# Kernel optimization log

Measured on AMD Instinct MI355X. Metric: run time of the kernel, lower is better.

The kernel has to match this reference:

```python
import jax, jax.numpy as jnp
import numpy as np

EPS = 1.0        # model eps for norm
STEP = 0.05      # step_size

def _norm(x):
    # torch: x / (eps + x.std(-1, keepdims=True)), torch std is unbiased (ddof=1)
    return x / (EPS + jnp.std(x, axis=-1, keepdims=True, ddof=1))

def setup_inputs() -> dict:
    key = jax.random.key(0)
    B, L, LM = 4, 512, 64
    G, E, K, D, KN = 32000, 256, 8, 6, 4
    ks = jax.random.split(key, 16)
    s = lambda k, shape, fan: (jax.random.normal(k, shape, jnp.float32) / np.sqrt(fan)).astype(jnp.float32)
    return dict(
        masked=jax.random.randint(ks[0], (B, L), 0, G),
        unmasked=jax.random.randint(ks[1], (B, L), 0, G),
        mask=jax.random.randint(ks[2], (B, LM), 0, L),
        embed=s(ks[3], (G, E), E),                 # embedding table
        Wt=s(ks[4], (D, E, E), E),                 # transition.weight per layer
        bt=jnp.zeros((D, E), jnp.float32),         # transition.bias per layer
        Wtc=s(ks[5], (D, E, E), E),                # transcore.weight per layer
        Wq=s(ks[6], (D, K * E, E), E),             # attq.weight per layer
        Wd=s(ks[7], (D, K * E, K * E), K * E),     # att_dense.weight per layer
        Wo=s(ks[8], (D, K * E, E), K * E),         # atto.weight per layer
        Wu=s(ks[9], (D, E, E), E),                 # updater.weight per layer
        Wem=s(ks[10], (E, E), E),                  # emittor.weight (head)
        Wkc=s(ks[11], (E * KN, E), E),             # kchoice.weight (head)
        bkc=jnp.zeros((E * KN,), jnp.float32),     # kchoice.bias (head)
    )

def reference(masked, unmasked, mask, embed, Wt, bt, Wtc, Wq, Wd, Wo, Wu, Wem, Wkc, bkc):
    B, L = masked.shape
    G, E = embed.shape
    K = Wq.shape[1] // E
    KN = Wkc.shape[0] // E
    inv_sqrt_e = 1.0 / np.sqrt(E)

    z = _norm(embed[masked])          # [B,L,E] input image
    xsa0 = z

    def step(xsa, p):
        wt, bt_, wtc, wq, wd, wo, wu = p
        # roll-based left/right transitions
        xsad = jax.nn.relu(jnp.roll(xsa, 1, axis=1) @ wt) @ wtc
        xsad = xsad + jax.nn.relu(jnp.roll(xsa, -1, axis=1) @ wtc.T) @ wt.T
        xsad = xsad + z @ wu.T + bt_   # use_input_image
        # QKV_Attention with kernel-expanded head dim: q [B,L,K,E] vs keys/values xsa [B,L,E]
        q = (xsa @ wq.T).reshape(B, L, K, E)
        h = jnp.einsum('blke,bme->blkm', q, xsa) * inv_sqrt_e
        pijk = jax.nn.softmax(h, axis=-1)
        y = jnp.einsum('blkm,bme->blke', pijk, xsa).reshape(B, L, K * E)
        # mode 1: Dense -> Relu -> Dense
        xid = jax.nn.relu(y @ wd.T) @ wo     # [B,L,E]
        xsad = _norm(xsad + xid)             # use_gradnorm
        xsa = _norm(xsa + STEP * xsad)       # use_layernorm
        return xsa, None

    xsa, _ = jax.lax.scan(step, xsa0, (Wt, bt, Wtc, Wq, Wd, Wo, Wu))

    # k-choice loss head (callback_cent)
    LM = mask.shape[1]
    lptok = jnp.take_along_axis(xsa, mask[:, :, None], axis=1)         # [B,LM,E]
    xx = (lptok @ Wkc.T + bkc).reshape(B, LM * KN, E)                  # kchoice
    xx = jnp.einsum('bnl,ble->bne', jnp.einsum('bne,ble->bnl', xx, xsa), xsa)
    logits = (xx @ Wem) @ embed.T                                      # [B,LM*KN,G]
    k_lp = jax.nn.log_softmax(logits, axis=-1).reshape(B, LM, KN, G)
    lptok = jax.scipy.special.logsumexp(k_lp, axis=2) - jnp.log(jnp.float32(KN))
    tgt = jnp.take_along_axis(unmasked, mask, axis=1)                  # [B,LM]
    cent = jnp.take_along_axis(lptok, tgt[:, :, None], axis=-1)[:, :, 0]
    return -cent.mean(-1)                                              # [B]
```

## Files before the change

kernel.cpp:

```cpp
#include <hip/hip_runtime.h>
#include <hip/hip_bf16.h>
#include <math.h>

typedef __bf16 bf16x8 __attribute__((ext_vector_type(8)));
typedef float floatx4 __attribute__((ext_vector_type(4)));

__device__ __forceinline__ short f2b(float f) {
  __hip_bfloat16 h = __float2bfloat16(f);
  return *reinterpret_cast<short*>(&h);
}
__device__ __forceinline__ float b2f(short s) {
  unsigned u = ((unsigned)(unsigned short)s) << 16;
  float f;
  __builtin_memcpy(&f, &u, 4);
  return f;
}

__device__ __forceinline__ void gl2lds16(const void* g, void* l) {
  __builtin_amdgcn_global_load_lds((__attribute__((address_space(1))) const void*)g,
                                   (__attribute__((address_space(3))) void*)l, 16, 0, 0);
}

__device__ __forceinline__ float block_sum(float v, float* sdata) {
#pragma unroll
  for (int o = 32; o > 0; o >>= 1) v += __shfl_down(v, o, 64);
  __syncthreads();
  int lane = threadIdx.x & 63, wid = threadIdx.x >> 6;
  if (lane == 0) sdata[wid] = v;
  __syncthreads();
  float s = 0.f;
  int nw = blockDim.x >> 6;
  for (int i = 0; i < nw; i++) s += sdata[i];
  return s;
}

__global__ void cvt_kernel(const float* __restrict__ src, short* __restrict__ dst, long n4) {
  long i = (long)blockIdx.x * blockDim.x + threadIdx.x;
  if (i < n4) {
    float4 v = ((const float4*)src)[i];
    short4 o;
    o.x = f2b(v.x); o.y = f2b(v.y); o.z = f2b(v.z); o.w = f2b(v.w);
    ((short4*)dst)[i] = o;
  }
}

__global__ void cvt2_kernel(const float* __restrict__ src, short* __restrict__ dst,
                            int ldS, int ldD, long sS, long sD) {
  src += (size_t)blockIdx.z * sS;
  dst += (size_t)blockIdx.z * sD;
  int c = blockIdx.x * 32 + threadIdx.x;
  int r0 = blockIdx.y * 32 + threadIdx.y;
#pragma unroll
  for (int i = 0; i < 32; i += 8)
    dst[(size_t)(r0 + i) * ldD + c] = f2b(src[(size_t)(r0 + i) * ldS + c]);
}

__global__ void cvtT2_kernel(const float* __restrict__ src, short* __restrict__ dst,
                             int ldS, int ldD, long sS, long sD) {
  src += (size_t)blockIdx.z * sS;
  dst += (size_t)blockIdx.z * sD;
  __shared__ float tile[32][33];
  int r0 = blockIdx.y * 32, c0 = blockIdx.x * 32;
  int tx = threadIdx.x, ty = threadIdx.y;
#pragma unroll
  for (int i = 0; i < 32; i += 8)
    tile[ty + i][tx] = src[(size_t)(r0 + ty + i) * ldS + c0 + tx];
  __syncthreads();
#pragma unroll
  for (int i = 0; i < 32; i += 8)
    dst[(size_t)(c0 + ty + i) * ldD + r0 + tx] = f2b(tile[tx][ty + i]);
}

__global__ void embed_norm_kernel(const int* __restrict__ masked,
                                  const float* __restrict__ embed,
                                  float* __restrict__ xsa, short* __restrict__ xsa_bf,
                                  short* __restrict__ xsaT_bf, short* __restrict__ catA,
                                  int E, int L, int ldA, int zoff) {
  int row = blockIdx.x;
  int g = masked[row];
  __shared__ float sdata[8];
  float x = embed[(size_t)g * E + threadIdx.x];
  float mean = block_sum(x, sdata) / E;
  float d = x - mean;
  float var = block_sum(d * d, sdata) / (E - 1);
  float val = x / (1.0f + sqrtf(var));
  size_t off = (size_t)row * E + threadIdx.x;
  xsa[off] = val;
  short b = f2b(val);
  xsa_bf[off] = b;
  catA[(size_t)row * ldA + zoff + threadIdx.x] = b;
  int bb = row / L, l = row - bb * L;
  xsaT_bf[((size_t)bb * E + threadIdx.x) * L + l] = b;
}

template <int BM, int BN, int OUT_BF16, int ASUM>
__global__ __launch_bounds__(256) void bgemm_kernel(
    const short* __restrict__ A, int lda, long sA,
    const short* __restrict__ B, int ldb, long sB,
    void* __restrict__ Cv, int ldc, long sC,
    short* __restrict__ C2b, int ldc2, int ncut,
    int Ksz, float alpha, const float* __restrict__ bias,
    int relu, int expo, int shiftA, int shiftB, int ns1, int ns2, int Lroll,
    int ksplit, long ksC) {
  constexpr int WM = BM / 2, WN = BN / 2;
  constexpr int MT = WM / 16, NT = WN / 16;
  constexpr int NCH = (BM + BN) * 8;
  constexpr int LPT = NCH / 256;
  int bz = blockIdx.z, kz = 0;
  if (ksplit > 1) {
    bz = blockIdx.z / ksplit;
    kz = blockIdx.z - bz * ksplit;
  }
  int Kper = Ksz / ksplit;
  int koff = kz * Kper;
  A += (size_t)bz * sA + koff;
  B += (size_t)bz * sB + koff;
  float* Cf = (float*)Cv + (size_t)bz * sC + (size_t)kz * ksC;
  short* Cb = (short*)Cv + (size_t)bz * sC;
  int m0 = blockIdx.y * BM, n0 = blockIdx.x * BN;
  int shift = (n0 < ns1) ? shiftA : ((n0 < ns2) ? shiftB : 0);
  int zone2 = (C2b != nullptr) && (n0 >= ncut);
  __shared__ short S[2][(BM + BN) * 64];
  int tid = threadIdx.x, lane = tid & 63, w = tid >> 6;
  int wm = (w & 1) * WM, wn = (w >> 1) * WN;
  int ml = lane & 15, q4 = lane >> 4, sw = ml & 7;

  const short* src[LPT];
#pragma unroll
  for (int i = 0; i < LPT; i++) {
    int q = i * 256 + w * 64 + lane;
    if (q < BM * 8) {
      int m = q >> 3, cl = q & 7, cs = cl ^ (m & 7);
      int mg = m0 + m;
      if (shift != 0) {
        int bb = mg / Lroll, l = mg - bb * Lroll;
        l = (l + shift + Lroll) % Lroll;
        mg = bb * Lroll + l;
      }
      src[i] = A + (size_t)mg * lda + cs * 8;
    } else {
      int qb = q - BM * 8;
      int n = qb >> 3, cl = qb & 7, cs = cl ^ (n & 7);
      src[i] = B + (size_t)(n0 + n) * ldb + cs * 8;
    }
  }
#pragma unroll
  for (int i = 0; i < LPT; i++)
    gl2lds16(src[i], &S[0][(i * 256 + w * 64) * 8]);
  floatx4 acc[MT][NT] = {};
  floatx4 sumacc[ASUM ? MT : 1] = {};
  bf16x8 ones;
#pragma unroll
  for (int i = 0; i < 8; i++) ones[i] = (__bf16)1.0f;
  int nT = Kper >> 6;
  for (int t = 0; t < nT; t++) {
    __syncthreads();
    int cur = t & 1;
    if (t + 1 < nT) {
      int nxt = cur ^ 1, ko = (t + 1) * 64;
#pragma unroll
      for (int i = 0; i < LPT; i++)
        gl2lds16(src[i] + ko, &S[nxt][(i * 256 + w * 64) * 8]);
    }
#pragma unroll
    for (int kk = 0; kk < 2; kk++) {
      int j = kk * 4 + q4;
      bf16x8 af[MT], bg[NT];
#pragma unroll
      for (int mt = 0; mt < MT; mt++) {
        int r = wm + mt * 16 + ml;
        af[mt] = *reinterpret_cast<const bf16x8*>(&S[cur][r * 64 + (j ^ sw) * 8]);
      }
#pragma unroll
      for (int nt = 0; nt < NT; nt++) {
        int r = wn + nt * 16 + ml;
        bg[nt] = *reinterpret_cast<const bf16x8*>(&S[cur][BM * 64 + r * 64 + (j ^ sw) * 8]);
      }
#pragma unroll
      for (int mt = 0; mt < MT; mt++)
#pragma unroll
        for (int nt = 0; nt < NT; nt++)
          acc[mt][nt] = __builtin_amdgcn_mfma_f32_16x16x32_bf16(af[mt], bg[nt], acc[mt][nt], 0, 0, 0);
      if (ASUM)
#pragma unroll
        for (int mt = 0; mt < MT; mt++)
          sumacc[mt] = __builtin_amdgcn_mfma_f32_16x16x32_bf16(af[mt], ones, sumacc[mt], 0, 0, 0);
    }
  }
#pragma unroll
  for (int mt = 0; mt < MT; mt++) {
    float sinv[4];
    if (ASUM) {
#pragma unroll
      for (int r = 0; r < 4; r++) sinv[r] = 1.f / sumacc[mt][r];
    }
#pragma unroll
    for (int nt = 0; nt < NT; nt++) {
      floatx4 v = acc[mt][nt];
#pragma unroll
      for (int r = 0; r < 4; r++) {
        int grow = m0 + wm + mt * 16 + q4 * 4 + r;
        int gcol = n0 + wn + nt * 16 + ml;
        float x = alpha * v[r];
        if (ASUM) x *= sinv[r];
        if (bias && kz == 0) x += bias[gcol];
        if (relu && !zone2) x = fmaxf(x, 0.f);
        if (expo) x = exp2f(x);
        if (OUT_BF16) {
          if (zone2)
            C2b[(size_t)grow * ldc2 + (gcol - ncut)] = f2b(x);
          else
            Cb[(size_t)grow * ldc + gcol] = f2b(x);
        } else {
          Cf[(size_t)grow * ldc + gcol] = x;
        }
      }
    }
  }
}

__global__ void addnorm_kernel(const float* __restrict__ xA, const float* __restrict__ xB,
                               float* __restrict__ xsa, short* __restrict__ xsa_bf,
                               short* __restrict__ xsaT_bf, int E, int L) {
  int row = blockIdx.x, t = threadIdx.x;
  __shared__ float sdata[8];
  size_t off = (size_t)row * E + t;
  float s1 = xA[off] + xB[off];
  float mean = block_sum(s1, sdata) / E;
  float d = s1 - mean;
  float var = block_sum(d * d, sdata) / (E - 1);
  float n1 = s1 / (1.f + sqrtf(var));
  float t2 = xsa[off] + 0.05f * n1;
  float mean2 = block_sum(t2, sdata) / E;
  float d2 = t2 - mean2;
  float var2 = block_sum(d2 * d2, sdata) / (E - 1);
  float res = t2 / (1.f + sqrtf(var2));
  xsa[off] = res;
  short b = f2b(res);
  xsa_bf[off] = b;
  int bb = row / L, l = row - bb * L;
  xsaT_bf[((size_t)bb * E + t) * L + l] = b;
}

__global__ void gather_kernel(const float* __restrict__ xsa, const int* __restrict__ mask,
                              const int* __restrict__ unmasked,
                              short* __restrict__ lptok_bf, int* __restrict__ tgt,
                              int L, int LM, int E) {
  int bi = blockIdx.x;
  int b = bi / LM;
  int pos = mask[bi];
  float v = xsa[((size_t)b * L + pos) * E + threadIdx.x];
  lptok_bf[(size_t)bi * E + threadIdx.x] = f2b(v);
  if (threadIdx.x == 0) tgt[bi] = unmasked[b * L + pos];
}

__global__ __launch_bounds__(256) void head_stats_kernel(
    const short* __restrict__ V, const short* __restrict__ Eb,
    float* __restrict__ stM, float* __restrict__ stS, int Ksz, int nch) {
  int t0 = blockIdx.x;
  int xcd = t0 & 7, j = t0 >> 3;
  int c = ((j >> 3) << 3) | xcd;
  if (c >= nch) return;
  int m0 = (j & 7) * 128, n0 = c * 128;
  __shared__ short As[2][8192];
  __shared__ short Bs[2][8192];
  int tid = threadIdx.x, lane = tid & 63, w = tid >> 6;
  int wm = (w & 1) * 64, wn = (w >> 1) * 64;
  int ml = lane & 15, q4 = lane >> 4, sw = ml & 7;
  const short* aSrc[4];
  const short* bSrc[4];
#pragma unroll
  for (int i = 0; i < 4; i++) {
    int q = i * 256 + w * 64 + lane;
    int m = q >> 3, cl = q & 7;
    int cs = cl ^ (m & 7);
    aSrc[i] = V + (size_t)(m0 + m) * Ksz + cs * 8;
    bSrc[i] = Eb + (size_t)(n0 + m) * Ksz + cs * 8;
  }
#pragma unroll
  for (int i = 0; i < 4; i++) {
    gl2lds16(aSrc[i], &As[0][(i * 256 + w * 64) * 8]);
    gl2lds16(bSrc[i], &Bs[0][(i * 256 + w * 64) * 8]);
  }
  floatx4 acc[4][4] = {};
  int nT = Ksz >> 6;
  for (int t = 0; t < nT; t++) {
    __syncthreads();
    int cur = t & 1;
    if (t + 1 < nT) {
      int nxt = cur ^ 1, ko = (t + 1) * 64;
#pragma unroll
      for (int i = 0; i < 4; i++) {
        gl2lds16(aSrc[i] + ko, &As[nxt][(i * 256 + w * 64) * 8]);
        gl2lds16(bSrc[i] + ko, &Bs[nxt][(i * 256 + w * 64) * 8]);
      }
    }
#pragma unroll
    for (int kk = 0; kk < 2; kk++) {
      int j2 = kk * 4 + q4;
      bf16x8 af[4], bg[4];
#pragma unroll
      for (int mt = 0; mt < 4; mt++) {
        int r = wm + mt * 16 + ml;
        af[mt] = *reinterpret_cast<const bf16x8*>(&As[cur][r * 64 + (j2 ^ sw) * 8]);
      }
#pragma unroll
      for (int nt = 0; nt < 4; nt++) {
        int r = wn + nt * 16 + ml;
        bg[nt] = *reinterpret_cast<const bf16x8*>(&Bs[cur][r * 64 + (j2 ^ sw) * 8]);
      }
#pragma unroll
      for (int mt = 0; mt < 4; mt++)
#pragma unroll
        for (int nt = 0; nt < 4; nt++)
          acc[mt][nt] = __builtin_amdgcn_mfma_f32_16x16x32_bf16(af[mt], bg[nt], acc[mt][nt], 0, 0, 0);
    }
  }
  __syncthreads();
  const float log2e = 1.4426950408889634f;
  float (*sred)[2] = (float (*)[2]) & As[0][0];
  float (*sred2)[2] = (float (*)[2]) & Bs[0][0];
  float mx[4][4];
#pragma unroll
  for (int mt = 0; mt < 4; mt++)
#pragma unroll
    for (int r = 0; r < 4; r++)
      mx[mt][r] = fmaxf(fmaxf(acc[mt][0][r], acc[mt][1][r]), fmaxf(acc[mt][2][r], acc[mt][3][r]));
#pragma unroll
  for (int off = 1; off < 16; off <<= 1)
#pragma unroll
    for (int mt = 0; mt < 4; mt++)
#pragma unroll
      for (int r = 0; r < 4; r++) mx[mt][r] = fmaxf(mx[mt][r], __shfl_xor(mx[mt][r], off, 64));
  if (ml == 0)
#pragma unroll
    for (int mt = 0; mt < 4; mt++)
#pragma unroll
      for (int r = 0; r < 4; r++) sred[wm + mt * 16 + q4 * 4 + r][w >> 1] = mx[mt][r];
  __syncthreads();
  float sm[4][4];
#pragma unroll
  for (int mt = 0; mt < 4; mt++)
#pragma unroll
    for (int r = 0; r < 4; r++) {
      int row = wm + mt * 16 + q4 * 4 + r;
      float fm = fmaxf(sred[row][0], sred[row][1]);
      float s = 0.f;
#pragma unroll
      for (int nt = 0; nt < 4; nt++) s += exp2f((acc[mt][nt][r] - fm) * log2e);
      sm[mt][r] = s;
    }
#pragma unroll
  for (int off = 1; off < 16; off <<= 1)
#pragma unroll
    for (int mt = 0; mt < 4; mt++)
#pragma unroll
      for (int r = 0; r < 4; r++) sm[mt][r] += __shfl_xor(sm[mt][r], off, 64);
  if (ml == 0)
#pragma unroll
    for (int mt = 0; mt < 4; mt++)
#pragma unroll
      for (int r = 0; r < 4; r++) sred2[wm + mt * 16 + q4 * 4 + r][w >> 1] = sm[mt][r];
  __syncthreads();
  if (tid < 128) {
    float fm = fmaxf(sred[tid][0], sred[tid][1]);
    stM[(size_t)(m0 + tid) * nch + c] = fm;
    stS[(size_t)(m0 + tid) * nch + c] = sred2[tid][0] + sred2[tid][1];
  }
}

__global__ void lse_reduce_kernel(const float* __restrict__ statsM,
                                  const float* __restrict__ statsS,
                                  float* __restrict__ lse, int nch) {
  int row = blockIdx.x, t = threadIdx.x;
  float m = -INFINITY, s = 0.f;
  for (int c = t; c < nch; c += blockDim.x) {
    float cm = statsM[(size_t)row * nch + c];
    float cs = statsS[(size_t)row * nch + c];
    float M = fmaxf(m, cm);
    s = s * expf(m - M) + cs * expf(cm - M);
    m = M;
  }
  __shared__ float sm[256], ss[256];
  sm[t] = m;
  ss[t] = s;
  __syncthreads();
  for (int o = 128; o > 0; o >>= 1) {
    if (t < o) {
      float m2 = sm[t + o], s2 = ss[t + o];
      float M = fmaxf(sm[t], m2);
      float sc = ss[t] * expf(sm[t] - M) + s2 * expf(m2 - M);
      sm[t] = M;
      ss[t] = sc;
    }
    __syncthreads();
  }
  if (t == 0) lse[row] = sm[0] + logf(ss[0]);
}

__global__ void logit_tgt_kernel(const short* __restrict__ V, const short* __restrict__ Eb,
                                 const int* __restrict__ tgt, float* __restrict__ lt,
                                 int E, int Nn, int KN, int LM) {
  int row = blockIdx.x;
  int b = row / Nn;
  int i = (row - b * Nn) / KN;
  int g = tgt[b * LM + i];
  __shared__ float sdata[8];
  float v = b2f(V[(size_t)row * E + threadIdx.x]) * b2f(Eb[(size_t)g * E + threadIdx.x]);
  float s = block_sum(v, sdata);
  if (threadIdx.x == 0) lt[row] = s;
}

__global__ void final_kernel(const float* __restrict__ lt, const float* __restrict__ lse,
                             float* __restrict__ out, int LM, int KN) {
  int b = blockIdx.x, i = threadIdx.x;
  int base = (b * LM + i) * KN;
  float m = -INFINITY;
  for (int k = 0; k < KN; k++) m = fmaxf(m, lt[base + k] - lse[base + k]);
  float s = 0.f;
  for (int k = 0; k < KN; k++) s += expf(lt[base + k] - lse[base + k] - m);
  float cent = m + logf(s) - logf((float)KN);
#pragma unroll
  for (int o = 32; o > 0; o >>= 1) cent += __shfl_down(cent, o, 64);
  if (i == 0) out[b] = -cent / LM;
}

static inline void bgemm(hipStream_t st, int cfg, const short* A, int lda, long sA,
                         const short* B, int ldb, long sB,
                         void* C, int ldc, long sC, int M, int N, int Ksz, int nb,
                         float alpha, const float* bias, int relu, int out_bf16,
                         int shiftA, int shiftB, int ns1, int ns2, int Lroll,
                         int expo = 0, int asum = 0,
                         short* C2 = nullptr, int ldc2 = 0, int ncut = 0,
                         int ksplit = 1, long ksC = 0) {
  dim3 block(256);
  int nz = nb * ksplit;
#define BG_ARGS A, lda, sA, B, ldb, sB, C, ldc, sC, C2, ldc2, ncut, Ksz, alpha, bias, relu, expo, shiftA, shiftB, ns1, ns2, Lroll, ksplit, ksC
  if (cfg == 0) {
    dim3 grid(N / 128, M / 128, nz);
    if (out_bf16)
      bgemm_kernel<128, 128, 1, 0><<<grid, block, 0, st>>>(BG_ARGS);
    else
      bgemm_kernel<128, 128, 0, 0><<<grid, block, 0, st>>>(BG_ARGS);
  } else if (cfg == 1) {
    dim3 grid(N / 64, M / 128, nz);
    if (out_bf16) {
      if (asum)
        bgemm_kernel<128, 64, 1, 1><<<grid, block, 0, st>>>(BG_ARGS);
      else
        bgemm_kernel<128, 64, 1, 0><<<grid, block, 0, st>>>(BG_ARGS);
    } else {
      bgemm_kernel<128, 64, 0, 0><<<grid, block, 0, st>>>(BG_ARGS);
    }
  } else {
    dim3 grid(N / 64, M / 64, nz);
    if (out_bf16)
      bgemm_kernel<64, 64, 1, 0><<<grid, block, 0, st>>>(BG_ARGS);
    else
      bgemm_kernel<64, 64, 0, 0><<<grid, block, 0, st>>>(BG_ARGS);
  }
#undef BG_ARGS
}

static inline void cvt(hipStream_t st, const float* src, short* dst, long n) {
  long n4 = n / 4;
  cvt_kernel<<<(int)((n4 + 255) / 256), 256, 0, st>>>(src, dst, n4);
}

static inline void cvt2(hipStream_t st, const float* src, short* dst, int R, int C,
                        int ldS, int ldD, long sS, long sD, int nb) {
  dim3 grid(C / 32, R / 32, nb), block(32, 8);
  cvt2_kernel<<<grid, block, 0, st>>>(src, dst, ldS, ldD, sS, sD);
}

static inline void cvtT2(hipStream_t st, const float* src, short* dst, int R, int C,
                         int ldS, int ldD, long sS, long sD, int nb) {
  dim3 grid(C / 32, R / 32, nb), block(32, 8);
  cvtT2_kernel<<<grid, block, 0, st>>>(src, dst, ldS, ldD, sS, sD);
}

extern "C" void kernel_launch(void* const* d_in, const int* in_sizes, int n_in,
                              void* d_out, int out_size, void* d_ws, size_t ws_size,
                              hipStream_t stream) {
  const int* masked = (const int*)d_in[0];
  const int* unmasked = (const int*)d_in[1];
  const int* mask = (const int*)d_in[2];
  const float* embed = (const float*)d_in[3];
  const float* Wt = (const float*)d_in[4];
  const float* bt = (const float*)d_in[5];
  const float* Wtc = (const float*)d_in[6];
  const float* Wq = (const float*)d_in[7];
  const float* Wd = (const float*)d_in[8];
  const float* Wo = (const float*)d_in[9];
  const float* Wu = (const float*)d_in[10];
  const float* Wem = (const float*)d_in[11];
  const float* Wkc = (const float*)d_in[12];
  const float* bkc = (const float*)d_in[13];

  const int B = out_size;
  const int BL = in_sizes[0];
  const int L = BL / B;
  const int BLM = in_sizes[2];
  const int LM = BLM / B;
  const int E = in_sizes[4] / in_sizes[5];
  const int D = in_sizes[5] / E;
  const int G = in_sizes[3] / E;
  const int K = in_sizes[7] / (D * E * E);
  const int KN = in_sizes[12] / (E * E);
  const int KE = K * E;
  const int N = LM * KN;
  const float inv_sqrt_e = 1.0f / sqrtf((float)E);
  const int nch = G / 128;
  const int E3 = 3 * E;
  const int KA = E3 + KE;
  const int NQ = 2 * E + KE;

  char* base = (char*)d_ws;
  size_t off = 0;
  auto carve = [&](size_t bytes) {
    char* p = base + off;
    off += (bytes + 255) & ~(size_t)255;
    return p;
  };
  float* xsa = (float*)carve((size_t)BL * E * 4);
  float* xsad = (float*)carve((size_t)2 * BL * E * 4);
  float* stM = (float*)carve((size_t)B * N * nch * 4);
  float* stS = (float*)carve((size_t)B * N * nch * 4);
  float* lse = (float*)carve((size_t)B * N * 4);
  float* lt = (float*)carve((size_t)B * N * 4);
  int* tgt = (int*)carve((size_t)B * LM * 4);
  short* xsa_bf = (short*)carve((size_t)BL * E * 2);
  short* xsaT_bf = (short*)carve((size_t)B * E * L * 2);
  short* catA = (short*)carve((size_t)BL * KA * 2);
  short* qy_bf = (short*)carve((size_t)BL * KE * 2);
  short* hP_bf = (short*)carve((size_t)B * L * K * L * 2);
  short* wd_all = (short*)carve((size_t)D * KE * KE * 2);
  short* BcatQ = (short*)carve((size_t)D * NQ * E * 2);
  short* Bcat2x = (short*)carve((size_t)D * E * KA * 2);
  short* embed_bf = (short*)carve((size_t)G * E * 2);
  short* WemT_bf = (short*)carve((size_t)E * E * 2);
  short* Wkc_bf = (short*)carve((size_t)KN * E * E * 2);
  short* gram_bf = (short*)carve((size_t)B * E * E * 2);
  short* xx_bf = (short*)carve((size_t)B * N * E * 2);
  short* xx2_bf = (short*)carve((size_t)B * N * E * 2);
  short* vv_bf = (short*)carve((size_t)B * N * E * 2);
  short* lptok_bf = (short*)carve((size_t)BLM * E * 2);

  cvt(stream, embed, embed_bf, (long)G * E);
  cvt(stream, Wd, wd_all, (long)D * KE * KE);
  cvt(stream, Wkc, Wkc_bf, (long)KN * E * E);
  cvtT2(stream, Wem, WemT_bf, E, E, E, E, 0, 0, 1);
  cvtT2(stream, Wt, BcatQ, E, E, E, E, (long)E * E, (long)NQ * E, D);
  cvt2(stream, Wtc, BcatQ + (size_t)E * E, E, E, E, E, (long)E * E, (long)NQ * E, D);
  cvt2(stream, Wq, BcatQ + (size_t)2 * E * E, KE, E, E, E, (long)KE * E, (long)NQ * E, D);
  cvtT2(stream, Wtc, Bcat2x, E, E, E, KA, (long)E * E, (long)E * KA, D);
  cvt2(stream, Wt, Bcat2x + E, E, E, E, KA, (long)E * E, (long)E * KA, D);
  cvt2(stream, Wu, Bcat2x + 2 * E, E, E, E, KA, (long)E * E, (long)E * KA, D);
  cvtT2(stream, Wo, Bcat2x + E3, KE, E, E, KA, (long)KE * E, (long)E * KA, D);

  embed_norm_kernel<<<BL, E, 0, stream>>>(masked, embed, xsa, xsa_bf, xsaT_bf, catA,
                                          E, L, KA, 2 * E);

  const float log2e = 1.4426950408889634f;
  for (int d = 0; d < D; d++) {
    const float* btl = bt + (size_t)d * E;
    bgemm(stream, 1, xsa_bf, E, 0, BcatQ + (size_t)d * NQ * E, E, 0,
          catA, KA, 0, BL, NQ, E, 1, 1.f, nullptr, 1, 1,
          -1, +1, E, 2 * E, L, 0, 0, qy_bf, KE, 2 * E);
    bgemm(stream, 0, qy_bf, E, (long)L * KE, xsa_bf, E, (long)L * E,
          hP_bf, L, (long)L * K * L, L * K, L, E, B, inv_sqrt_e * log2e, nullptr, 0, 1,
          0, 0, 0, 0, L, 1);
    bgemm(stream, 1, hP_bf, L, (long)L * K * L, xsaT_bf, L, (long)E * L,
          qy_bf, E, (long)L * KE, L * K, E, L, B, 1.f, nullptr, 0, 1,
          0, 0, 0, 0, L, 0, 1);
    bgemm(stream, 0, qy_bf, KE, 0, wd_all + (size_t)d * KE * KE, KE, 0,
          catA + E3, KA, 0, BL, KE, KE, 1, 1.f, nullptr, 1, 1, 0, 0, 0, 0, L);
    bgemm(stream, 2, catA, KA, 0, Bcat2x + (size_t)d * E * KA, KA, 0,
          xsad, E, 0, BL, E, KA, 1, 1.f, btl, 0, 0, 0, 0, 0, 0, L,
          0, 0, nullptr, 0, 0, 2, (long)BL * E);
    addnorm_kernel<<<BL, E, 0, stream>>>(xsad, xsad + (size_t)BL * E,
                                         xsa, xsa_bf, xsaT_bf, E, L);
  }

  gather_kernel<<<BLM, E, 0, stream>>>(xsa, mask, unmasked, lptok_bf, tgt, L, LM, E);
  bgemm(stream, 2, xsaT_bf, L, (long)E * L, xsaT_bf, L, (long)E * L,
        gram_bf, E, (long)E * E, E, E, L, B, 1.f, nullptr, 0, 1, 0, 0, 0, 0, L);
  bgemm(stream, 2, lptok_bf, E, 0, Wkc_bf, E, 0, xx_bf, KN * E, 0, BLM, KN * E, E, 1,
        1.f, bkc, 0, 1, 0, 0, 0, 0, L);
  bgemm(stream, 2, xx_bf, E, (long)N * E, gram_bf, E, (long)E * E,
        xx2_bf, E, (long)N * E, N, E, E, B, 1.f, nullptr, 0, 1, 0, 0, 0, 0, L);
  bgemm(stream, 2, xx2_bf, E, 0, WemT_bf, E, 0, vv_bf, E, 0, B * N, E, E, 1,
        1.f, nullptr, 0, 1, 0, 0, 0, 0, L);
  {
    int nchPad = (nch + 7) & ~7;
    head_stats_kernel<<<nchPad * 8, 256, 0, stream>>>(vv_bf, embed_bf, stM, stS, E, nch);
  }
  lse_reduce_kernel<<<B * N, 256, 0, stream>>>(stM, stS, lse, nch);
  logit_tgt_kernel<<<B * N, E, 0, stream>>>(vv_bf, embed_bf, tgt, lt, E, N, KN, LM);
  final_kernel<<<B, LM, 0, stream>>>(lt, lse, (float*)d_out, LM, KN);
}
```

Before: 908.0 us.

## Shrink head stats M-tile to 64 rows and transpose stats layout

```diff
diff --git a/kernel.cpp b/kernel.cpp
--- a/kernel.cpp
+++ b/kernel.cpp
@@ -256,33 +256,33 @@
 
 __global__ __launch_bounds__(256) void head_stats_kernel(
     const short* __restrict__ V, const short* __restrict__ Eb,
-    float* __restrict__ stM, float* __restrict__ stS, int Ksz, int nch) {
+    float* __restrict__ stM, float* __restrict__ stS, int Ksz, int nch, int Mrows) {
   int t0 = blockIdx.x;
   int xcd = t0 & 7, j = t0 >> 3;
-  int c = ((j >> 3) << 3) | xcd;
+  int c = ((j >> 4) << 3) | xcd;
   if (c >= nch) return;
-  int m0 = (j & 7) * 128, n0 = c * 128;
-  __shared__ short As[2][8192];
-  __shared__ short Bs[2][8192];
+  int m0 = (j & 15) * 64, n0 = c * 128;
+  __shared__ short S[2][(64 + 128) * 64];
   int tid = threadIdx.x, lane = tid & 63, w = tid >> 6;
-  int wm = (w & 1) * 64, wn = (w >> 1) * 64;
+  int wm = (w & 1) * 32, wn = (w >> 1) * 64;
   int ml = lane & 15, q4 = lane >> 4, sw = ml & 7;
-  const short* aSrc[4];
-  const short* bSrc[4];
-#pragma unroll
-  for (int i = 0; i < 4; i++) {
+  const short* src[6];
+#pragma unroll
+  for (int i = 0; i < 6; i++) {
     int q = i * 256 + w * 64 + lane;
-    int m = q >> 3, cl = q & 7;
-    int cs = cl ^ (m & 7);
-    aSrc[i] = V + (size_t)(m0 + m) * Ksz + cs * 8;
-    bSrc[i] = Eb + (size_t)(n0 + m) * Ksz + cs * 8;
-  }
-#pragma unroll
-  for (int i = 0; i < 4; i++) {
-    gl2lds16(aSrc[i], &As[0][(i * 256 + w * 64) * 8]);
-    gl2lds16(bSrc[i], &Bs[0][(i * 256 + w * 64) * 8]);
-  }
-  floatx4 acc[4][4] = {};
+    if (q < 512) {
+      int m = q >> 3, cl = q & 7, cs = cl ^ (m & 7);
+      src[i] = V + (size_t)(m0 + m) * Ksz + cs * 8;
+    } else {
+      int qb = q - 512;
+      int n = qb >> 3, cl = qb & 7, cs = cl ^ (n & 7);
+      src[i] = Eb + (size_t)(n0 + n) * Ksz + cs * 8;
+    }
+  }
+#pragma unroll
+  for (int i = 0; i < 6; i++)
+    gl2lds16(src[i], &S[0][(i * 256 + w * 64) * 8]);
+  floatx4 acc[2][4] = {};
   int nT = Ksz >> 6;
   for (int t = 0; t < nT; t++) {
     __syncthreads();
@@ -290,27 +290,25 @@
     if (t + 1 < nT) {
       int nxt = cur ^ 1, ko = (t + 1) * 64;
 #pragma unroll
-      for (int i = 0; i < 4; i++) {
-        gl2lds16(aSrc[i] + ko, &As[nxt][(i * 256 + w * 64) * 8]);
-        gl2lds16(bSrc[i] + ko, &Bs[nxt][(i * 256 + w * 64) * 8]);
-      }
+      for (int i = 0; i < 6; i++)
+        gl2lds16(src[i] + ko, &S[nxt][(i * 256 + w * 64) * 8]);
     }
 #pragma unroll
     for (int kk = 0; kk < 2; kk++) {
-      int j2 = kk * 4 + q4;
-      bf16x8 af[4], bg[4];
-#pragma unroll
-      for (int mt = 0; mt < 4; mt++) {
+      int jj = kk * 4 + q4;
+      bf16x8 af[2], bg[4];
+#pragma unroll
+      for (int mt = 0; mt < 2; mt++) {
         int r = wm + mt * 16 + ml;
-        af[mt] = *reinterpret_cast<const bf16x8*>(&As[cur][r * 64 + (j2 ^ sw) * 8]);
+        af[mt] = *reinterpret_cast<const bf16x8*>(&S[cur][r * 64 + (jj ^ sw) * 8]);
       }
 #pragma unroll
       for (int nt = 0; nt < 4; nt++) {
         int r = wn + nt * 16 + ml;
-        bg[nt] = *reinterpret_cast<const bf16x8*>(&Bs[cur][r * 64 + (j2 ^ sw) * 8]);
+        bg[nt] = *reinterpret_cast<const bf16x8*>(&S[cur][512 * 8 + r * 64 + (jj ^ sw) * 8]);
       }
 #pragma unroll
-      for (int mt = 0; mt < 4; mt++)
+      for (int mt = 0; mt < 2; mt++)
 #pragma unroll
         for (int nt = 0; nt < 4; nt++)
           acc[mt][nt] = __builtin_amdgcn_mfma_f32_16x16x32_bf16(af[mt], bg[nt], acc[mt][nt], 0, 0, 0);
@@ -318,29 +316,29 @@
   }
   __syncthreads();
   const float log2e = 1.4426950408889634f;
-  float (*sred)[2] = (float (*)[2]) & As[0][0];
-  float (*sred2)[2] = (float (*)[2]) & Bs[0][0];
-  float mx[4][4];
-#pragma unroll
-  for (int mt = 0; mt < 4; mt++)
+  float (*sred)[2] = (float (*)[2]) & S[0][0];
+  float (*sred2)[2] = (float (*)[2]) & S[1][0];
+  float mx[2][4];
+#pragma unroll
+  for (int mt = 0; mt < 2; mt++)
 #pragma unroll
     for (int r = 0; r < 4; r++)
       mx[mt][r] = fmaxf(fmaxf(acc[mt][0][r], acc[mt][1][r]), fmaxf(acc[mt][2][r], acc[mt][3][r]));
 #pragma unroll
   for (int off = 1; off < 16; off <<= 1)
 #pragma unroll
-    for (int mt = 0; mt < 4; mt++)
+    for (int mt = 0; mt < 2; mt++)
 #pragma unroll
       for (int r = 0; r < 4; r++) mx[mt][r] = fmaxf(mx[mt][r], __shfl_xor(mx[mt][r], off, 64));
   if (ml == 0)
 #pragma unroll
-    for (int mt = 0; mt < 4; mt++)
+    for (int mt = 0; mt < 2; mt++)
 #pragma unroll
       for (int r = 0; r < 4; r++) sred[wm + mt * 16 + q4 * 4 + r][w >> 1] = mx[mt][r];
   __syncthreads();
-  float sm[4][4];
-#pragma unroll
-  for (int mt = 0; mt < 4; mt++)
+  float sm[2][4];
+#pragma unroll
+  for (int mt = 0; mt < 2; mt++)
 #pragma unroll
     for (int r = 0; r < 4; r++) {
       int row = wm + mt * 16 + q4 * 4 + r;
@@ -353,30 +351,30 @@
 #pragma unroll
   for (int off = 1; off < 16; off <<= 1)
 #pragma unroll
-    for (int mt = 0; mt < 4; mt++)
+    for (int mt = 0; mt < 2; mt++)
 #pragma unroll
       for (int r = 0; r < 4; r++) sm[mt][r] += __shfl_xor(sm[mt][r], off, 64);
   if (ml == 0)
 #pragma unroll
-    for (int mt = 0; mt < 4; mt++)
+    for (int mt = 0; mt < 2; mt++)
 #pragma unroll
       for (int r = 0; r < 4; r++) sred2[wm + mt * 16 + q4 * 4 + r][w >> 1] = sm[mt][r];
   __syncthreads();
-  if (tid < 128) {
+  if (tid < 64) {
     float fm = fmaxf(sred[tid][0], sred[tid][1]);
-    stM[(size_t)(m0 + tid) * nch + c] = fm;
-    stS[(size_t)(m0 + tid) * nch + c] = sred2[tid][0] + sred2[tid][1];
+    stM[(size_t)c * Mrows + m0 + tid] = fm;
+    stS[(size_t)c * Mrows + m0 + tid] = sred2[tid][0] + sred2[tid][1];
   }
 }
 
 __global__ void lse_reduce_kernel(const float* __restrict__ statsM,
                                   const float* __restrict__ statsS,
-                                  float* __restrict__ lse, int nch) {
+                                  float* __restrict__ lse, int nch, int Mrows) {
   int row = blockIdx.x, t = threadIdx.x;
   float m = -INFINITY, s = 0.f;
   for (int c = t; c < nch; c += blockDim.x) {
-    float cm = statsM[(size_t)row * nch + c];
-    float cs = statsS[(size_t)row * nch + c];
+    float cm = statsM[(size_t)c * Mrows + row];
+    float cs = statsS[(size_t)c * Mrows + row];
     float M = fmaxf(m, cm);
     s = s * expf(m - M) + cs * expf(cm - M);
     m = M;
@@ -593,9 +591,10 @@
         1.f, nullptr, 0, 1, 0, 0, 0, 0, L);
   {
     int nchPad = (nch + 7) & ~7;
-    head_stats_kernel<<<nchPad * 8, 256, 0, stream>>>(vv_bf, embed_bf, stM, stS, E, nch);
-  }
-  lse_reduce_kernel<<<B * N, 256, 0, stream>>>(stM, stS, lse, nch);
+    head_stats_kernel<<<nchPad * 16, 256, 0, stream>>>(vv_bf, embed_bf, stM, stS,
+                                                       E, nch, B * N);
+  }
+  lse_reduce_kernel<<<B * N, 256, 0, stream>>>(stM, stS, lse, nch, B * N);
   logit_tgt_kernel<<<B * N, E, 0, stream>>>(vv_bf, embed_bf, tgt, lt, E, N, KN, LM);
   final_kernel<<<B, LM, 0, stream>>>(lt, lse, (float*)d_out, LM, KN);
 }
```

Result: faster. 889.7 us (-2.0%).
